# Kernel optimization log

Measured on AMD Instinct MI355X. Metric: run time of the kernel, lower is better.

The kernel has to match this reference:

```python
import jax, jax.numpy as jnp
import numpy as np

B, N, D, H, W = 8, 4096, 256, 64, 64  # N must equal H*W for the Z normalization einsum


def setup_inputs() -> dict:
    key = jax.random.key(0)
    ks = jax.random.split(key, 10)
    s = 1.0 / np.sqrt(D)
    return {
        "query": jax.random.normal(ks[0], (B, N, D), jnp.float32),
        "key_value": jax.random.normal(ks[1], (B, D, H, W), jnp.float32),
        "Wq": jax.random.uniform(ks[2], (D, D), jnp.float32, -s, s),
        "bq": jax.random.uniform(ks[3], (D,), jnp.float32, -s, s),
        "Wk": jax.random.uniform(ks[4], (D, D), jnp.float32, -s, s),
        "bk": jax.random.uniform(ks[5], (D,), jnp.float32, -s, s),
        "Wv": jax.random.uniform(ks[6], (D, D), jnp.float32, -s, s),
        "bv": jax.random.uniform(ks[7], (D,), jnp.float32, -s, s),
        "Wo": jax.random.uniform(ks[8], (D, D), jnp.float32, -s, s),
        "bo": jax.random.uniform(ks[9], (D,), jnp.float32, -s, s),
    }


def reference(query, key_value, Wq, bq, Wk, bk, Wv, bv, Wo, bo):
    b, n, d = query.shape
    # [B, C, H, W] -> [B, HW, C]
    kv_flat = key_value.reshape(b, d, -1).transpose(0, 2, 1)
    # projections (torch Linear: x @ W.T + b) fused with elu+1 feature maps
    Q = jax.nn.elu(jnp.einsum('bnd,ed->bne', query, Wq) + bq) + 1.0   # [B, N, D]
    K = jax.nn.elu(jnp.einsum('bmd,ed->bme', kv_flat, Wk) + bk) + 1.0  # [B, HW, D]
    V = jnp.einsum('bmd,ed->bme', kv_flat, Wv) + bv                    # [B, HW, D]
    # KV outer-product accumulation over kv tokens
    KV = jnp.einsum('bmc,bmd->bcd', K, V)                              # [B, D, D]
    # Z[b,m] = sum_c K[b,m,c]  (used per-token; requires N == HW)
    Z = K.sum(axis=-1)                                                 # [B, N]
    num = jnp.einsum('bnc,bcd->bnd', Q, KV)                            # [B, N, D]
    den = Q.sum(axis=-1) * Z                                           # [B, N]
    out = num / (den[..., None] + 1e-6)
    return jnp.einsum('bnd,ed->bne', out, Wo) + bo
```

## Files before the change

kernel.cpp:

```cpp
#include <hip/hip_runtime.h>
#include <hip/hip_bf16.h>


typedef __attribute__((ext_vector_type(8))) __bf16 bf16x8;
typedef __attribute__((ext_vector_type(4))) float f32x4;
typedef __attribute__((ext_vector_type(4))) unsigned short u16x4;
typedef __attribute__((ext_vector_type(8))) unsigned short u16x8;

#define DEVI __device__ __forceinline__

static constexpr int BATCH = 8;
static constexpr int NTOK  = 4096;
static constexpr int DDIM  = 256;

DEVI float bf2f(unsigned short u) {
  union { float f; unsigned int i; } x; x.i = ((unsigned int)u) << 16; return x.f;
}
DEVI unsigned short f2bf(float f) {
  union { float f; unsigned int i; } x; x.f = f;
  unsigned int r = x.i + 0x7fffu + ((x.i >> 16) & 1u);
  return (unsigned short)(r >> 16);
}

__global__ __launch_bounds__(256) void conv_q_kernel(const float* __restrict__ src,
                                                     unsigned short* __restrict__ dst) {
  size_t base = ((size_t)blockIdx.x * 256 + threadIdx.x) * 16;
#pragma unroll
  for (int j = 0; j < 4; ++j) {
    float4 v = *reinterpret_cast<const float4*>(src + base + j * 4);
    u16x4 o = { f2bf(v.x), f2bf(v.y), f2bf(v.z), f2bf(v.w) };
    *reinterpret_cast<u16x4*>(dst + base + j * 4) = o;
  }
}

__global__ __launch_bounds__(256) void conv_w_kernel(const float* __restrict__ w0, const float* __restrict__ w1,
                                                     const float* __restrict__ w2, const float* __restrict__ w3,
                                                     unsigned short* __restrict__ o0, unsigned short* __restrict__ o1,
                                                     unsigned short* __restrict__ o2, unsigned short* __restrict__ o3) {
  size_t i = ((size_t)blockIdx.x * 256 + threadIdx.x) * 4;
  float4 a = *reinterpret_cast<const float4*>(w0 + i);
  float4 b = *reinterpret_cast<const float4*>(w1 + i);
  float4 c = *reinterpret_cast<const float4*>(w2 + i);
  float4 d = *reinterpret_cast<const float4*>(w3 + i);
  u16x4 oa = { f2bf(a.x), f2bf(a.y), f2bf(a.z), f2bf(a.w) };
  u16x4 ob = { f2bf(b.x), f2bf(b.y), f2bf(b.z), f2bf(b.w) };
  u16x4 oc = { f2bf(c.x), f2bf(c.y), f2bf(c.z), f2bf(c.w) };
  u16x4 od = { f2bf(d.x), f2bf(d.y), f2bf(d.z), f2bf(d.w) };
  *reinterpret_cast<u16x4*>(o0 + i) = oa;
  *reinterpret_cast<u16x4*>(o1 + i) = ob;
  *reinterpret_cast<u16x4*>(o2 + i) = oc;
  *reinterpret_cast<u16x4*>(o3 + i) = od;
}

__global__ __launch_bounds__(256) void kv_transpose(const float* __restrict__ src,
                                                    unsigned short* __restrict__ dst) {
  __shared__ float t[32][33];
  int b = blockIdx.z;
  int m0 = blockIdx.x * 32, d0 = blockIdx.y * 32;
  int tx = threadIdx.x, ty = threadIdx.y;
  const float* s = src + ((size_t)b * DDIM + d0) * NTOK + m0;
#pragma unroll
  for (int i = 0; i < 4; ++i) t[ty + i * 8][tx] = s[(size_t)(ty + i * 8) * NTOK + tx];
  __syncthreads();
  unsigned short* d = dst + ((size_t)b * NTOK + m0) * DDIM + d0;
#pragma unroll
  for (int i = 0; i < 4; ++i) d[(size_t)(ty + i * 8) * DDIM + tx] = f2bf(t[tx][ty + i * 8]);
}

__global__ __launch_bounds__(256) void t64_kernel(const unsigned short* __restrict__ src,
                                                  unsigned short* __restrict__ dst) {
  constexpr int LDT = 68;
  __shared__ unsigned short Ts[64 * LDT];
  const int tid = threadIdx.x;
  const int b = blockIdx.z;
  const int m0 = blockIdx.x * 64;
  const int c0 = blockIdx.y * 64;
  {
    const int cg = tid & 15;
    const int rb = tid >> 4;
#pragma unroll
    for (int it = 0; it < 4; ++it) {
      int r = rb + it * 16;
      u16x4 v = *reinterpret_cast<const u16x4*>(src + ((size_t)b * NTOK + m0 + r) * 256 + c0 + cg * 4);
      *reinterpret_cast<u16x4*>(&Ts[r * LDT + cg * 4]) = v;
    }
  }
  __syncthreads();
  {
    const int c = tid >> 2;
    const int mg = tid & 3;
    u16x8 o0, o1;
#pragma unroll
    for (int j = 0; j < 8; ++j) o0[j] = Ts[(mg * 16 + j) * LDT + c];
#pragma unroll
    for (int j = 0; j < 8; ++j) o1[j] = Ts[(mg * 16 + 8 + j) * LDT + c];
    unsigned short* d = dst + ((size_t)b * DDIM + c0 + c) * NTOK + m0 + mg * 16;
    *reinterpret_cast<u16x8*>(d) = o0;
    *reinterpret_cast<u16x8*>(d + 8) = o1;
  }
}

template <int ACT>
__global__ __launch_bounds__(256) void gemm_proj(const unsigned short* __restrict__ A,
                                                 const unsigned short* __restrict__ W,
                                                 const float* __restrict__ bias,
                                                 unsigned short* __restrict__ outp) {
  constexpr int LDT = 72;
  __shared__ unsigned short As[128 * LDT];
  __shared__ unsigned short Ws[128 * LDT];

  const int tid = threadIdx.x;
  const int m0 = blockIdx.x * 128;
  const int c0 = blockIdx.y * 128;
  const int w = tid >> 6, l = tid & 63;
  const int wr = (w >> 1) * 64, wc = (w & 1) * 64;
  const int lr = l & 15, lk = (l >> 4) * 8;

  f32x4 acc[4][4] = {};

  for (int k0 = 0; k0 < 256; k0 += 64) {
#pragma unroll
    for (int it = 0; it < 4; ++it) {
      int idx = tid + it * 256;
      int r = idx >> 3;
      int c = (idx & 7) * 8;
      *reinterpret_cast<u16x8*>(&As[r * LDT + c]) =
          *reinterpret_cast<const u16x8*>(A + (size_t)(m0 + r) * 256 + k0 + c);
      *reinterpret_cast<u16x8*>(&Ws[r * LDT + c]) =
          *reinterpret_cast<const u16x8*>(W + (size_t)(c0 + r) * 256 + k0 + c);
    }
    __syncthreads();
#pragma unroll
    for (int kk = 0; kk < 2; ++kk) {
      bf16x8 a[4], b[4];
#pragma unroll
      for (int m = 0; m < 4; ++m)
        a[m] = *reinterpret_cast<const bf16x8*>(&As[(wr + m * 16 + lr) * LDT + kk * 32 + lk]);
#pragma unroll
      for (int n = 0; n < 4; ++n)
        b[n] = *reinterpret_cast<const bf16x8*>(&Ws[(wc + n * 16 + lr) * LDT + kk * 32 + lk]);
#pragma unroll
      for (int m = 0; m < 4; ++m)
#pragma unroll
        for (int n = 0; n < 4; ++n)
          acc[m][n] = __builtin_amdgcn_mfma_f32_16x16x32_bf16(a[m], b[n], acc[m][n], 0, 0, 0);
    }
    __syncthreads();
  }

#pragma unroll
  for (int n = 0; n < 4; ++n) {
    const int col = c0 + wc + n * 16 + lr;
    const float bv = bias[col];
#pragma unroll
    for (int m = 0; m < 4; ++m) {
#pragma unroll
      for (int j = 0; j < 4; ++j) {
        int row = m0 + wr + m * 16 + (l >> 4) * 4 + j;
        float x = acc[m][n][j] + bv;
        if (ACT) x = (x > 0.0f) ? (x + 1.0f) : __expf(x);
        outp[(size_t)row * 256 + col] = f2bf(x);
      }
    }
  }
}

__global__ __launch_bounds__(256) void den_kernel(const unsigned short* __restrict__ Qb,
                                                  const unsigned short* __restrict__ Kb,
                                                  float* __restrict__ den) {
  int row = blockIdx.x * 4 + (threadIdx.x >> 6);
  int l = threadIdx.x & 63;
  u16x4 q = *reinterpret_cast<const u16x4*>(Qb + (size_t)row * 256 + l * 4);
  u16x4 k = *reinterpret_cast<const u16x4*>(Kb + (size_t)row * 256 + l * 4);
  float qs = bf2f(q[0]) + bf2f(q[1]) + bf2f(q[2]) + bf2f(q[3]);
  float ks = bf2f(k[0]) + bf2f(k[1]) + bf2f(k[2]) + bf2f(k[3]);
#pragma unroll
  for (int s = 32; s > 0; s >>= 1) {
    qs += __shfl_xor(qs, s);
    ks += __shfl_xor(ks, s);
  }
  if (l == 0) den[row] = qs * ks;
}

__global__ __launch_bounds__(256) void kv_gemm(const unsigned short* __restrict__ Kt,
                                               const unsigned short* __restrict__ Vt,
                                               float* __restrict__ partial) {
  constexpr int LDT = 72;
  __shared__ unsigned short As[128 * LDT];
  __shared__ unsigned short Bs[128 * LDT];
  const int tid = threadIdx.x;
  const int b = blockIdx.z;
  const int s = blockIdx.y;
  const int ct0 = (blockIdx.x >> 1) * 128;
  const int dt0 = (blockIdx.x & 1) * 128;
  const int ms = s * 512;

  const int w = tid >> 6, l = tid & 63;
  const int wr = (w >> 1) * 64, wc = (w & 1) * 64;
  const int lr = l & 15, lk = (l >> 4) * 8;

  const size_t kbase = ((size_t)b * DDIM + ct0) * NTOK;
  const size_t vbase = ((size_t)b * DDIM + dt0) * NTOK;

  f32x4 acc[4][4] = {};

  for (int mc = 0; mc < 512; mc += 64) {
#pragma unroll
    for (int it = 0; it < 4; ++it) {
      int idx = tid + it * 256;
      int r = idx >> 3;
      int kg = (idx & 7) * 8;
      *reinterpret_cast<u16x8*>(&As[r * LDT + kg]) =
          *reinterpret_cast<const u16x8*>(Kt + kbase + (size_t)r * NTOK + ms + mc + kg);
      *reinterpret_cast<u16x8*>(&Bs[r * LDT + kg]) =
          *reinterpret_cast<const u16x8*>(Vt + vbase + (size_t)r * NTOK + ms + mc + kg);
    }
    __syncthreads();
#pragma unroll
    for (int kk = 0; kk < 2; ++kk) {
      bf16x8 a[4], bb[4];
#pragma unroll
      for (int m = 0; m < 4; ++m)
        a[m] = *reinterpret_cast<const bf16x8*>(&As[(wr + m * 16 + lr) * LDT + kk * 32 + lk]);
#pragma unroll
      for (int n = 0; n < 4; ++n)
        bb[n] = *reinterpret_cast<const bf16x8*>(&Bs[(wc + n * 16 + lr) * LDT + kk * 32 + lk]);
#pragma unroll
      for (int m = 0; m < 4; ++m)
#pragma unroll
        for (int n = 0; n < 4; ++n)
          acc[m][n] = __builtin_amdgcn_mfma_f32_16x16x32_bf16(a[m], bb[n], acc[m][n], 0, 0, 0);
    }
    __syncthreads();
  }

  float* p = partial + (size_t)(s * BATCH + b) * 65536;
#pragma unroll
  for (int n = 0; n < 4; ++n) {
    int d = dt0 + wc + n * 16 + lr;
#pragma unroll
    for (int m = 0; m < 4; ++m) {
#pragma unroll
      for (int j = 0; j < 4; ++j) {
        int c = ct0 + wr + m * 16 + (l >> 4) * 4 + j;
        p[(size_t)c * 256 + d] = acc[m][n][j];
      }
    }
  }
}

__global__ __launch_bounds__(256) void kv_reduce(const float* __restrict__ partial,
                                                 unsigned short* __restrict__ KVb) {
  size_t i = ((size_t)blockIdx.x * 256 + threadIdx.x) * 4;
  float4 acc = *reinterpret_cast<const float4*>(partial + i);
#pragma unroll
  for (int s = 1; s < 8; ++s) {
    float4 v = *reinterpret_cast<const float4*>(partial + (size_t)s * 524288 + i);
    acc.x += v.x; acc.y += v.y; acc.z += v.z; acc.w += v.w;
  }
  u16x4 o = { f2bf(acc.x), f2bf(acc.y), f2bf(acc.z), f2bf(acc.w) };
  *reinterpret_cast<u16x4*>(KVb + i) = o;
}

__global__ __launch_bounds__(256) void w2_gemm(const unsigned short* __restrict__ wob,
                                               const unsigned short* __restrict__ KVb,
                                               unsigned short* __restrict__ W2T) {
  constexpr int LDT = 72;
  __shared__ unsigned short As[128 * LDT];
  __shared__ unsigned short Bs[128 * LDT];
  const int tid = threadIdx.x;
  const int b = blockIdx.z;
  const int e0 = blockIdx.x * 128;
  const int c0 = blockIdx.y * 128;
  const unsigned short* Bsrc = KVb + (size_t)b * 65536;

  const int w = tid >> 6, l = tid & 63;
  const int wr = (w >> 1) * 64, wc = (w & 1) * 64;
  const int lr = l & 15, lk = (l >> 4) * 8;

  f32x4 acc[4][4] = {};

  for (int k0 = 0; k0 < 256; k0 += 64) {
#pragma unroll
    for (int it = 0; it < 4; ++it) {
      int idx = tid + it * 256;
      int r = idx >> 3;
      int c = (idx & 7) * 8;
      *reinterpret_cast<u16x8*>(&As[r * LDT + c]) =
          *reinterpret_cast<const u16x8*>(wob + (size_t)(e0 + r) * 256 + k0 + c);
      *reinterpret_cast<u16x8*>(&Bs[r * LDT + c]) =
          *reinterpret_cast<const u16x8*>(Bsrc + (size_t)(c0 + r) * 256 + k0 + c);
    }
    __syncthreads();
#pragma unroll
    for (int kk = 0; kk < 2; ++kk) {
      bf16x8 a[4], bb[4];
#pragma unroll
      for (int m = 0; m < 4; ++m)
        a[m] = *reinterpret_cast<const bf16x8*>(&As[(wr + m * 16 + lr) * LDT + kk * 32 + lk]);
#pragma unroll
      for (int n = 0; n < 4; ++n)
        bb[n] = *reinterpret_cast<const bf16x8*>(&Bs[(wc + n * 16 + lr) * LDT + kk * 32 + lk]);
#pragma unroll
      for (int m = 0; m < 4; ++m)
#pragma unroll
        for (int n = 0; n < 4; ++n)
          acc[m][n] = __builtin_amdgcn_mfma_f32_16x16x32_bf16(a[m], bb[n], acc[m][n], 0, 0, 0);
    }
    __syncthreads();
  }

  unsigned short* out = W2T + (size_t)b * 65536;
#pragma unroll
  for (int n = 0; n < 4; ++n) {
    int c = c0 + wc + n * 16 + lr;
#pragma unroll
    for (int m = 0; m < 4; ++m) {
#pragma unroll
      for (int j = 0; j < 4; ++j) {
        int e = e0 + wr + m * 16 + (l >> 4) * 4 + j;
        out[(size_t)e * 256 + c] = f2bf(acc[m][n][j]);
      }
    }
  }
}

__global__ __launch_bounds__(256) void gemm_final(const unsigned short* __restrict__ Qb,
                                                  const unsigned short* __restrict__ W2T,
                                                  const float* __restrict__ den,
                                                  const float* __restrict__ bo,
                                                  float* __restrict__ outp) {
  constexpr int LDT = 72;
  __shared__ unsigned short As[128 * LDT];
  __shared__ unsigned short Bs[128 * LDT];
  const int tid = threadIdx.x;
  const int b = blockIdx.z;
  const int m0 = blockIdx.x * 128;
  const int e0 = blockIdx.y * 128;
  const size_t abase = (size_t)b * NTOK;
  const unsigned short* Bsrc = W2T + (size_t)b * 65536;

  const int w = tid >> 6, l = tid & 63;
  const int wr = (w >> 1) * 64, wc = (w & 1) * 64;
  const int lr = l & 15, lk = (l >> 4) * 8;

  f32x4 acc[4][4] = {};

  for (int k0 = 0; k0 < 256; k0 += 64) {
#pragma unroll
    for (int it = 0; it < 4; ++it) {
      int idx = tid + it * 256;
      int r = idx >> 3, c = (idx & 7) * 8;
      *reinterpret_cast<u16x8*>(&As[r * LDT + c]) =
          *reinterpret_cast<const u16x8*>(Qb + (abase + m0 + r) * 256 + k0 + c);
      *reinterpret_cast<u16x8*>(&Bs[r * LDT + c]) =
          *reinterpret_cast<const u16x8*>(Bsrc + (size_t)(e0 + r) * 256 + k0 + c);
    }
    __syncthreads();
#pragma unroll
    for (int kk = 0; kk < 2; ++kk) {
      bf16x8 a[4], bb[4];
#pragma unroll
      for (int m = 0; m < 4; ++m)
        a[m] = *reinterpret_cast<const bf16x8*>(&As[(wr + m * 16 + lr) * LDT + kk * 32 + lk]);
#pragma unroll
      for (int n = 0; n < 4; ++n)
        bb[n] = *reinterpret_cast<const bf16x8*>(&Bs[(wc + n * 16 + lr) * LDT + kk * 32 + lk]);
#pragma unroll
      for (int m = 0; m < 4; ++m)
#pragma unroll
        for (int n = 0; n < 4; ++n)
          acc[m][n] = __builtin_amdgcn_mfma_f32_16x16x32_bf16(a[m], bb[n], acc[m][n], 0, 0, 0);
    }
    __syncthreads();
  }

#pragma unroll
  for (int n = 0; n < 4; ++n) {
    int col = e0 + wc + n * 16 + lr;
    const float bv = bo[col];
#pragma unroll
    for (int m = 0; m < 4; ++m) {
#pragma unroll
      for (int j = 0; j < 4; ++j) {
        int row = m0 + wr + m * 16 + (l >> 4) * 4 + j;
        float dv = den[abase + row] + 1e-6f;
        outp[(abase + row) * 256 + col] = acc[m][n][j] / dv + bv;
      }
    }
  }
}

extern "C" void kernel_launch(void* const* d_in, const int* in_sizes, int n_in,
                              void* d_out, int out_size, void* d_ws, size_t ws_size,
                              hipStream_t stream) {
  const float* query     = (const float*)d_in[0];
  const float* key_value = (const float*)d_in[1];
  const float* Wq = (const float*)d_in[2];
  const float* bq = (const float*)d_in[3];
  const float* Wk = (const float*)d_in[4];
  const float* bk = (const float*)d_in[5];
  const float* Wv = (const float*)d_in[6];
  const float* bv = (const float*)d_in[7];
  const float* Wo = (const float*)d_in[8];
  const float* bo = (const float*)d_in[9];

  char* ws = (char*)d_ws;
  const size_t MB = 1ull << 20;
  unsigned short* q_bf  = (unsigned short*)(ws + 0 * MB);
  unsigned short* kv_bf = (unsigned short*)(ws + 16 * MB);
  unsigned short* Qb    = (unsigned short*)(ws + 32 * MB);
  unsigned short* Kb    = (unsigned short*)(ws + 48 * MB);
  unsigned short* Vb    = (unsigned short*)(ws + 64 * MB);
  unsigned short* KVb   = (unsigned short*)(ws + 80 * MB);
  unsigned short* W2T   = (unsigned short*)(ws + 81 * MB);
  float* den            = (float*)(ws + 82 * MB);
  unsigned short* wqb   = (unsigned short*)(ws + 82 * MB + 128 * 1024);
  unsigned short* wkb   = (unsigned short*)(ws + 82 * MB + 256 * 1024);
  unsigned short* wvb   = (unsigned short*)(ws + 82 * MB + 384 * 1024);
  unsigned short* wob   = (unsigned short*)(ws + 82 * MB + 512 * 1024);
  unsigned short* Kt    = q_bf;
  unsigned short* Vt    = kv_bf;
  float* partial        = (float*)(ws + 64 * MB);

  conv_q_kernel<<<2048, 256, 0, stream>>>(query, q_bf);
  conv_w_kernel<<<64, 256, 0, stream>>>(Wq, Wk, Wv, Wo, wqb, wkb, wvb, wob);
  kv_transpose<<<dim3(128, 8, 8), dim3(32, 8), 0, stream>>>(key_value, kv_bf);

  gemm_proj<1><<<dim3(256, 2), 256, 0, stream>>>(q_bf, wqb, bq, Qb);
  gemm_proj<1><<<dim3(256, 2), 256, 0, stream>>>(kv_bf, wkb, bk, Kb);
  gemm_proj<0><<<dim3(256, 2), 256, 0, stream>>>(kv_bf, wvb, bv, Vb);

  t64_kernel<<<dim3(64, 4, 8), 256, 0, stream>>>(Kb, Kt);
  t64_kernel<<<dim3(64, 4, 8), 256, 0, stream>>>(Vb, Vt);

  den_kernel<<<8192, 256, 0, stream>>>(Qb, Kb, den);
  kv_gemm<<<dim3(4, 8, 8), 256, 0, stream>>>(Kt, Vt, partial);
  kv_reduce<<<512, 256, 0, stream>>>(partial, KVb);
  w2_gemm<<<dim3(2, 2, 8), 256, 0, stream>>>(wob, KVb, W2T);

  gemm_final<<<dim3(32, 2, 8), 256, 0, stream>>>(Qb, W2T, den, bo, (float*)d_out);
}
```

Measured before the change: 256.5 us.

## Fuse bf16 conversion, transposes, and row-sum denominators into projection GEMMs

```diff
diff --git a/kernel.cpp b/kernel.cpp
--- a/kernel.cpp
+++ b/kernel.cpp
@@ -20,17 +20,6 @@
   union { float f; unsigned int i; } x; x.f = f;
   unsigned int r = x.i + 0x7fffu + ((x.i >> 16) & 1u);
   return (unsigned short)(r >> 16);
-}
-
-__global__ __launch_bounds__(256) void conv_q_kernel(const float* __restrict__ src,
-                                                     unsigned short* __restrict__ dst) {
-  size_t base = ((size_t)blockIdx.x * 256 + threadIdx.x) * 16;
-#pragma unroll
-  for (int j = 0; j < 4; ++j) {
-    float4 v = *reinterpret_cast<const float4*>(src + base + j * 4);
-    u16x4 o = { f2bf(v.x), f2bf(v.y), f2bf(v.z), f2bf(v.w) };
-    *reinterpret_cast<u16x4*>(dst + base + j * 4) = o;
-  }
 }
 
 __global__ __launch_bounds__(256) void conv_w_kernel(const float* __restrict__ w0, const float* __restrict__ w1,
@@ -67,44 +56,11 @@
   for (int i = 0; i < 4; ++i) d[(size_t)(ty + i * 8) * DDIM + tx] = f2bf(t[tx][ty + i * 8]);
 }
 
-__global__ __launch_bounds__(256) void t64_kernel(const unsigned short* __restrict__ src,
-                                                  unsigned short* __restrict__ dst) {
-  constexpr int LDT = 68;
-  __shared__ unsigned short Ts[64 * LDT];
-  const int tid = threadIdx.x;
-  const int b = blockIdx.z;
-  const int m0 = blockIdx.x * 64;
-  const int c0 = blockIdx.y * 64;
-  {
-    const int cg = tid & 15;
-    const int rb = tid >> 4;
-#pragma unroll
-    for (int it = 0; it < 4; ++it) {
-      int r = rb + it * 16;
-      u16x4 v = *reinterpret_cast<const u16x4*>(src + ((size_t)b * NTOK + m0 + r) * 256 + c0 + cg * 4);
-      *reinterpret_cast<u16x4*>(&Ts[r * LDT + cg * 4]) = v;
-    }
-  }
-  __syncthreads();
-  {
-    const int c = tid >> 2;
-    const int mg = tid & 3;
-    u16x8 o0, o1;
-#pragma unroll
-    for (int j = 0; j < 8; ++j) o0[j] = Ts[(mg * 16 + j) * LDT + c];
-#pragma unroll
-    for (int j = 0; j < 8; ++j) o1[j] = Ts[(mg * 16 + 8 + j) * LDT + c];
-    unsigned short* d = dst + ((size_t)b * DDIM + c0 + c) * NTOK + m0 + mg * 16;
-    *reinterpret_cast<u16x8*>(d) = o0;
-    *reinterpret_cast<u16x8*>(d + 8) = o1;
-  }
-}
-
-template <int ACT>
-__global__ __launch_bounds__(256) void gemm_proj(const unsigned short* __restrict__ A,
-                                                 const unsigned short* __restrict__ W,
-                                                 const float* __restrict__ bias,
-                                                 unsigned short* __restrict__ outp) {
+__global__ __launch_bounds__(256) void gemm_projq(const float* __restrict__ A,
+                                                  const unsigned short* __restrict__ W,
+                                                  const float* __restrict__ bias,
+                                                  unsigned short* __restrict__ Qb,
+                                                  float* __restrict__ qsum) {
   constexpr int LDT = 72;
   __shared__ unsigned short As[128 * LDT];
   __shared__ unsigned short Ws[128 * LDT];
@@ -124,8 +80,12 @@
       int idx = tid + it * 256;
       int r = idx >> 3;
       int c = (idx & 7) * 8;
-      *reinterpret_cast<u16x8*>(&As[r * LDT + c]) =
-          *reinterpret_cast<const u16x8*>(A + (size_t)(m0 + r) * 256 + k0 + c);
+      const float* s = A + (size_t)(m0 + r) * 256 + k0 + c;
+      float4 v0 = *reinterpret_cast<const float4*>(s);
+      float4 v1 = *reinterpret_cast<const float4*>(s + 4);
+      u16x8 o = { f2bf(v0.x), f2bf(v0.y), f2bf(v0.z), f2bf(v0.w),
+                  f2bf(v1.x), f2bf(v1.y), f2bf(v1.z), f2bf(v1.w) };
+      *reinterpret_cast<u16x8*>(&As[r * LDT + c]) = o;
       *reinterpret_cast<u16x8*>(&Ws[r * LDT + c]) =
           *reinterpret_cast<const u16x8*>(W + (size_t)(c0 + r) * 256 + k0 + c);
     }
@@ -148,6 +108,7 @@
     __syncthreads();
   }
 
+  float rsum[4][4] = {};
 #pragma unroll
   for (int n = 0; n < 4; ++n) {
     const int col = c0 + wc + n * 16 + lr;
@@ -158,28 +119,162 @@
       for (int j = 0; j < 4; ++j) {
         int row = m0 + wr + m * 16 + (l >> 4) * 4 + j;
         float x = acc[m][n][j] + bv;
-        if (ACT) x = (x > 0.0f) ? (x + 1.0f) : __expf(x);
-        outp[(size_t)row * 256 + col] = f2bf(x);
-      }
-    }
-  }
-}
-
-__global__ __launch_bounds__(256) void den_kernel(const unsigned short* __restrict__ Qb,
-                                                  const unsigned short* __restrict__ Kb,
-                                                  float* __restrict__ den) {
-  int row = blockIdx.x * 4 + (threadIdx.x >> 6);
-  int l = threadIdx.x & 63;
-  u16x4 q = *reinterpret_cast<const u16x4*>(Qb + (size_t)row * 256 + l * 4);
-  u16x4 k = *reinterpret_cast<const u16x4*>(Kb + (size_t)row * 256 + l * 4);
-  float qs = bf2f(q[0]) + bf2f(q[1]) + bf2f(q[2]) + bf2f(q[3]);
-  float ks = bf2f(k[0]) + bf2f(k[1]) + bf2f(k[2]) + bf2f(k[3]);
-#pragma unroll
-  for (int s = 32; s > 0; s >>= 1) {
-    qs += __shfl_xor(qs, s);
-    ks += __shfl_xor(ks, s);
-  }
-  if (l == 0) den[row] = qs * ks;
+        x = (x > 0.0f) ? (x + 1.0f) : __expf(x);
+        unsigned short h = f2bf(x);
+        Qb[(size_t)row * 256 + col] = h;
+        rsum[m][j] += bf2f(h);
+      }
+    }
+  }
+#pragma unroll
+  for (int mask = 1; mask < 16; mask <<= 1)
+#pragma unroll
+    for (int m = 0; m < 4; ++m)
+#pragma unroll
+      for (int j = 0; j < 4; ++j) rsum[m][j] += __shfl_xor(rsum[m][j], mask);
+  if (lr == 0) {
+#pragma unroll
+    for (int m = 0; m < 4; ++m)
+#pragma unroll
+      for (int j = 0; j < 4; ++j)
+        atomicAdd(&qsum[m0 + wr + m * 16 + (l >> 4) * 4 + j], rsum[m][j]);
+  }
+}
+
+__global__ __launch_bounds__(256) void gemm_projkv(const unsigned short* __restrict__ A,
+                                                   const unsigned short* __restrict__ Wk,
+                                                   const unsigned short* __restrict__ Wv,
+                                                   const float* __restrict__ bk,
+                                                   const float* __restrict__ bv,
+                                                   unsigned short* __restrict__ Kt,
+                                                   unsigned short* __restrict__ Vt,
+                                                   float* __restrict__ ksum) {
+  constexpr int LDT = 72;
+  constexpr int LDX = 136;
+  __shared__ unsigned short Smem[3 * 128 * LDT];
+  unsigned short* As  = Smem;
+  unsigned short* WsK = Smem + 128 * LDT;
+  unsigned short* WsV = Smem + 2 * 128 * LDT;
+  unsigned short* Tb  = Smem;
+
+  const int tid = threadIdx.x;
+  const int m0 = blockIdx.x * 128;
+  const int c0 = blockIdx.y * 128;
+  const int b = m0 >> 12;
+  const int mloc = m0 & 4095;
+  const int w = tid >> 6, l = tid & 63;
+  const int wr = (w >> 1) * 64, wc = (w & 1) * 64;
+  const int lr = l & 15, lk = (l >> 4) * 8;
+
+  f32x4 acck[4][4] = {}, accv[4][4] = {};
+
+  for (int k0 = 0; k0 < 256; k0 += 64) {
+#pragma unroll
+    for (int it = 0; it < 4; ++it) {
+      int idx = tid + it * 256;
+      int r = idx >> 3;
+      int c = (idx & 7) * 8;
+      *reinterpret_cast<u16x8*>(&As[r * LDT + c]) =
+          *reinterpret_cast<const u16x8*>(A + (size_t)(m0 + r) * 256 + k0 + c);
+      *reinterpret_cast<u16x8*>(&WsK[r * LDT + c]) =
+          *reinterpret_cast<const u16x8*>(Wk + (size_t)(c0 + r) * 256 + k0 + c);
+      *reinterpret_cast<u16x8*>(&WsV[r * LDT + c]) =
+          *reinterpret_cast<const u16x8*>(Wv + (size_t)(c0 + r) * 256 + k0 + c);
+    }
+    __syncthreads();
+#pragma unroll
+    for (int kk = 0; kk < 2; ++kk) {
+      bf16x8 a[4], fk[4], fv[4];
+#pragma unroll
+      for (int m = 0; m < 4; ++m)
+        a[m] = *reinterpret_cast<const bf16x8*>(&As[(wr + m * 16 + lr) * LDT + kk * 32 + lk]);
+#pragma unroll
+      for (int n = 0; n < 4; ++n) {
+        fk[n] = *reinterpret_cast<const bf16x8*>(&WsK[(wc + n * 16 + lr) * LDT + kk * 32 + lk]);
+        fv[n] = *reinterpret_cast<const bf16x8*>(&WsV[(wc + n * 16 + lr) * LDT + kk * 32 + lk]);
+      }
+#pragma unroll
+      for (int m = 0; m < 4; ++m)
+#pragma unroll
+        for (int n = 0; n < 4; ++n) {
+          acck[m][n] = __builtin_amdgcn_mfma_f32_16x16x32_bf16(a[m], fk[n], acck[m][n], 0, 0, 0);
+          accv[m][n] = __builtin_amdgcn_mfma_f32_16x16x32_bf16(a[m], fv[n], accv[m][n], 0, 0, 0);
+        }
+    }
+    __syncthreads();
+  }
+
+  float rsum[4][4] = {};
+#pragma unroll
+  for (int n = 0; n < 4; ++n) {
+    const int col = wc + n * 16 + lr;
+    const float bb = bk[c0 + col];
+#pragma unroll
+    for (int m = 0; m < 4; ++m) {
+      const int rb = wr + m * 16 + (l >> 4) * 4;
+#pragma unroll
+      for (int jj = 0; jj < 2; ++jj) {
+        float x0 = acck[m][n][2 * jj] + bb;     x0 = (x0 > 0.0f) ? (x0 + 1.0f) : __expf(x0);
+        float x1 = acck[m][n][2 * jj + 1] + bb; x1 = (x1 > 0.0f) ? (x1 + 1.0f) : __expf(x1);
+        unsigned short h0 = f2bf(x0), h1 = f2bf(x1);
+        rsum[m][2 * jj] += bf2f(h0);
+        rsum[m][2 * jj + 1] += bf2f(h1);
+        *reinterpret_cast<unsigned int*>(&Tb[(size_t)col * LDX + rb + 2 * jj]) =
+            (unsigned int)h0 | ((unsigned int)h1 << 16);
+      }
+    }
+  }
+#pragma unroll
+  for (int mask = 1; mask < 16; mask <<= 1)
+#pragma unroll
+    for (int m = 0; m < 4; ++m)
+#pragma unroll
+      for (int j = 0; j < 4; ++j) rsum[m][j] += __shfl_xor(rsum[m][j], mask);
+  if (lr == 0) {
+#pragma unroll
+    for (int m = 0; m < 4; ++m)
+#pragma unroll
+      for (int j = 0; j < 4; ++j)
+        atomicAdd(&ksum[m0 + wr + m * 16 + (l >> 4) * 4 + j], rsum[m][j]);
+  }
+  __syncthreads();
+  {
+    const int cl = tid >> 1;
+    const int mg = (tid & 1) * 64;
+    unsigned short* dst = Kt + ((size_t)b * DDIM + c0 + cl) * NTOK + mloc + mg;
+#pragma unroll
+    for (int k2 = 0; k2 < 8; ++k2)
+      *reinterpret_cast<u16x8*>(dst + k2 * 8) =
+          *reinterpret_cast<const u16x8*>(&Tb[(size_t)cl * LDX + mg + k2 * 8]);
+  }
+  __syncthreads();
+
+#pragma unroll
+  for (int n = 0; n < 4; ++n) {
+    const int col = wc + n * 16 + lr;
+    const float bb = bv[c0 + col];
+#pragma unroll
+    for (int m = 0; m < 4; ++m) {
+      const int rb = wr + m * 16 + (l >> 4) * 4;
+#pragma unroll
+      for (int jj = 0; jj < 2; ++jj) {
+        unsigned short h0 = f2bf(accv[m][n][2 * jj] + bb);
+        unsigned short h1 = f2bf(accv[m][n][2 * jj + 1] + bb);
+        *reinterpret_cast<unsigned int*>(&Tb[(size_t)col * LDX + rb + 2 * jj]) =
+            (unsigned int)h0 | ((unsigned int)h1 << 16);
+      }
+    }
+  }
+  __syncthreads();
+  {
+    const int cl = tid >> 1;
+    const int mg = (tid & 1) * 64;
+    unsigned short* dst = Vt + ((size_t)b * DDIM + c0 + cl) * NTOK + mloc + mg;
+#pragma unroll
+    for (int k2 = 0; k2 < 8; ++k2)
+      *reinterpret_cast<u16x8*>(dst + k2 * 8) =
+          *reinterpret_cast<const u16x8*>(&Tb[(size_t)cl * LDX + mg + k2 * 8]);
+  }
 }
 
 __global__ __launch_bounds__(256) void kv_gemm(const unsigned short* __restrict__ Kt,
@@ -327,7 +422,8 @@
 
 __global__ __launch_bounds__(256) void gemm_final(const unsigned short* __restrict__ Qb,
                                                   const unsigned short* __restrict__ W2T,
-                                                  const float* __restrict__ den,
+                                                  const float* __restrict__ qsum,
+                                                  const float* __restrict__ ksum,
                                                   const float* __restrict__ bo,
                                                   float* __restrict__ outp) {
   constexpr int LDT = 72;
@@ -378,14 +474,15 @@
 #pragma unroll
   for (int n = 0; n < 4; ++n) {
     int col = e0 + wc + n * 16 + lr;
-    const float bv = bo[col];
+    const float bb = bo[col];
 #pragma unroll
     for (int m = 0; m < 4; ++m) {
 #pragma unroll
       for (int j = 0; j < 4; ++j) {
         int row = m0 + wr + m * 16 + (l >> 4) * 4 + j;
-        float dv = den[abase + row] + 1e-6f;
-        outp[(abase + row) * 256 + col] = acc[m][n][j] / dv + bv;
+        size_t g = abase + row;
+        float dv = qsum[g] * ksum[g] + 1e-6f;
+        outp[g * 256 + col] = acc[m][n][j] / dv + bb;
       }
     }
   }
@@ -407,37 +504,31 @@
 
   char* ws = (char*)d_ws;
   const size_t MB = 1ull << 20;
-  unsigned short* q_bf  = (unsigned short*)(ws + 0 * MB);
-  unsigned short* kv_bf = (unsigned short*)(ws + 16 * MB);
-  unsigned short* Qb    = (unsigned short*)(ws + 32 * MB);
-  unsigned short* Kb    = (unsigned short*)(ws + 48 * MB);
-  unsigned short* Vb    = (unsigned short*)(ws + 64 * MB);
+  unsigned short* kv_bf = (unsigned short*)(ws + 0 * MB);
+  unsigned short* Qb    = (unsigned short*)(ws + 16 * MB);
+  unsigned short* Kt    = (unsigned short*)(ws + 32 * MB);
+  unsigned short* Vt    = (unsigned short*)(ws + 48 * MB);
+  float* partial        = (float*)(ws + 64 * MB);
   unsigned short* KVb   = (unsigned short*)(ws + 80 * MB);
   unsigned short* W2T   = (unsigned short*)(ws + 81 * MB);
-  float* den            = (float*)(ws + 82 * MB);
-  unsigned short* wqb   = (unsigned short*)(ws + 82 * MB + 128 * 1024);
-  unsigned short* wkb   = (unsigned short*)(ws + 82 * MB + 256 * 1024);
-  unsigned short* wvb   = (unsigned short*)(ws + 82 * MB + 384 * 1024);
-  unsigned short* wob   = (unsigned short*)(ws + 82 * MB + 512 * 1024);
-  unsigned short* Kt    = q_bf;
-  unsigned short* Vt    = kv_bf;
-  float* partial        = (float*)(ws + 64 * MB);
-
-  conv_q_kernel<<<2048, 256, 0, stream>>>(query, q_bf);
+  float* qsum           = (float*)(ws + 82 * MB);
+  float* ksum           = (float*)(ws + 82 * MB + 128 * 1024);
+  unsigned short* wqb   = (unsigned short*)(ws + 82 * MB + 256 * 1024);
+  unsigned short* wkb   = (unsigned short*)(ws + 82 * MB + 384 * 1024);
+  unsigned short* wvb   = (unsigned short*)(ws + 82 * MB + 512 * 1024);
+  unsigned short* wob   = (unsigned short*)(ws + 82 * MB + 640 * 1024);
+
+  hipMemsetAsync(qsum, 0, 2 * 128 * 1024, stream);
+
   conv_w_kernel<<<64, 256, 0, stream>>>(Wq, Wk, Wv, Wo, wqb, wkb, wvb, wob);
   kv_transpose<<<dim3(128, 8, 8), dim3(32, 8), 0, stream>>>(key_value, kv_bf);
 
-  gemm_proj<1><<<dim3(256, 2), 256, 0, stream>>>(q_bf, wqb, bq, Qb);
-  gemm_proj<1><<<dim3(256, 2), 256, 0, stream>>>(kv_bf, wkb, bk, Kb);
-  gemm_proj<0><<<dim3(256, 2), 256, 0, stream>>>(kv_bf, wvb, bv, Vb);
-
-  t64_kernel<<<dim3(64, 4, 8), 256, 0, stream>>>(Kb, Kt);
-  t64_kernel<<<dim3(64, 4, 8), 256, 0, stream>>>(Vb, Vt);
-
-  den_kernel<<<8192, 256, 0, stream>>>(Qb, Kb, den);
+  gemm_projq<<<dim3(256, 2), 256, 0, stream>>>(query, wqb, bq, Qb, qsum);
+  gemm_projkv<<<dim3(256, 2), 256, 0, stream>>>(kv_bf, wkb, wvb, bk, bv, Kt, Vt, ksum);
+
   kv_gemm<<<dim3(4, 8, 8), 256, 0, stream>>>(Kt, Vt, partial);
   kv_reduce<<<512, 256, 0, stream>>>(partial, KVb);
   w2_gemm<<<dim3(2, 2, 8), 256, 0, stream>>>(wob, KVb, W2T);
 
-  gemm_final<<<dim3(32, 2, 8), 256, 0, stream>>>(Qb, W2T, den, bo, (float*)d_out);
-}
+  gemm_final<<<dim3(32, 2, 8), 256, 0, stream>>>(Qb, W2T, qsum, ksum, bo, (float*)d_out);
+}
```

After: 225.5 us. 12.1% less time.
